# Kernel optimization log

Measured on AMD Instinct MI355X. Metric: run time of the kernel, lower is better.

## Reference

```python
import jax, jax.numpy as jnp
import numpy as np

CH = 64
GROUPS = 32
EPS = 1e-5


def setup_inputs() -> dict:
    key = jax.random.key(0)
    ks = jax.random.split(key, 10)
    b, c, h, w = 4, CH, 64, 64
    x = jax.random.normal(ks[0], (b, c, h, w), dtype=jnp.float32)
    s = 1.0 / np.sqrt(c)
    Wq = jax.random.normal(ks[1], (c, c), dtype=jnp.float32) * s
    bq = jnp.zeros((c,), dtype=jnp.float32)
    Wk = jax.random.normal(ks[2], (c, c), dtype=jnp.float32) * s
    bk = jnp.zeros((c,), dtype=jnp.float32)
    Wv = jax.random.normal(ks[3], (c, c), dtype=jnp.float32) * s
    bv = jnp.zeros((c,), dtype=jnp.float32)
    Wo = jax.random.normal(ks[4], (c, c), dtype=jnp.float32) * s
    bo = jnp.zeros((c,), dtype=jnp.float32)
    gamma = jnp.ones((c,), dtype=jnp.float32)
    beta = jnp.zeros((c,), dtype=jnp.float32)
    return {"x": x, "Wq": Wq, "bq": bq, "Wk": Wk, "bk": bk,
            "Wv": Wv, "bv": bv, "Wo": Wo, "bo": bo,
            "gamma": gamma, "beta": beta}


def group_norm(x, gamma, beta):
    b, c, h, w = x.shape
    xg = x.reshape(b, GROUPS, c // GROUPS, h, w)
    mean = jnp.mean(xg, axis=(2, 3, 4), keepdims=True)
    var = jnp.var(xg, axis=(2, 3, 4), keepdims=True)
    xn = ((xg - mean) * jax.lax.rsqrt(var + EPS)).reshape(b, c, h, w)
    return xn * gamma[None, :, None, None] + beta[None, :, None, None]


def conv1x1(x, W, bias):
    # 1x1 conv == channel matmul: x [b,c,h,w], W [out,in]
    return jnp.einsum('bchw,oc->bohw', x, W) + bias[None, :, None, None]


def reference(x, Wq, bq, Wk, bk, Wv, bv, Wo, bo, gamma, beta):
    b, c, h, w = x.shape
    n = h * w
    xn = group_norm(x, gamma, beta)
    q = conv1x1(xn, Wq, bq).reshape(b, c, n)  # [b,c,n]
    k = conv1x1(xn, Wk, bk).reshape(b, c, n)
    v = conv1x1(xn, Wv, bv).reshape(b, c, n)
    scale = 1.0 / jnp.sqrt(jnp.asarray(c, dtype=x.dtype))
    # scores: q^T k -> [b, n_q, n_k]
    attn = jax.nn.softmax(jnp.einsum('bci,bcj->bij', q, k) * scale, axis=-1)
    # out = v @ attn^T -> [b, c, n_q]
    out = jnp.einsum('bcj,bij->bci', v, attn).reshape(b, c, h, w)
    return x + conv1x1(out, Wo, bo)
```

## Files before the change

### kernel.cpp

```cpp
#include <hip/hip_runtime.h>
#include <hip/hip_bf16.h>

#define NPOS 4096
#define KS 72
#define VS 80

typedef __attribute__((ext_vector_type(4))) float f32x4;
typedef __attribute__((ext_vector_type(8))) short bf16x8;
typedef __attribute__((ext_vector_type(2))) int i32x2;
typedef _Float16 f16;
typedef __attribute__((ext_vector_type(8))) f16 f16x8;

__device__ __forceinline__ short f2bf(float f) {
  union { __hip_bfloat16 h; short s; } u;
  u.h = __float2bfloat16(f);
  return u.s;
}
__device__ __forceinline__ int pack_bf16(float lo, float hi) {
  unsigned a = (unsigned short)f2bf(lo);
  unsigned b = (unsigned short)f2bf(hi);
  return (int)(a | (b << 16));
}
__device__ __forceinline__ bf16x8 cvt8(const float* p) {
  f32x4 u = *(const f32x4*)p;
  f32x4 v = *(const f32x4*)(p + 4);
  bf16x8 r;
  r[0] = f2bf(u.x); r[1] = f2bf(u.y); r[2] = f2bf(u.z); r[3] = f2bf(u.w);
  r[4] = f2bf(v.x); r[5] = f2bf(v.y); r[6] = f2bf(v.z); r[7] = f2bf(v.w);
  return r;
}

__global__ __launch_bounds__(256) void stats_kernel(const float* __restrict__ x,
                                                    float* __restrict__ stats) {
  const int bg = blockIdx.x;
  const f32x4* base = (const f32x4*)(x + (size_t)bg * 8192);
  float s = 0.f, ss = 0.f;
  for (int i = threadIdx.x; i < 2048; i += 256) {
    f32x4 v = base[i];
    s  += v.x + v.y + v.z + v.w;
    ss += v.x * v.x + v.y * v.y + v.z * v.z + v.w * v.w;
  }
  for (int off = 32; off; off >>= 1) {
    s  += __shfl_down(s, off, 64);
    ss += __shfl_down(ss, off, 64);
  }
  __shared__ float red[8];
  const int wave = threadIdx.x >> 6, lane = threadIdx.x & 63;
  if (lane == 0) { red[wave] = s; red[4 + wave] = ss; }
  __syncthreads();
  if (threadIdx.x == 0) {
    float S  = red[0] + red[1] + red[2] + red[3];
    float SS = red[4] + red[5] + red[6] + red[7];
    float mean = S * (1.f / 8192.f);
    float var  = SS * (1.f / 8192.f) - mean * mean;
    stats[2 * bg]     = mean;
    stats[2 * bg + 1] = rsqrtf(var + 1e-5f);
  }
}

__global__ __launch_bounds__(256) void qkv_kernel(
    const float* __restrict__ x,
    const float* __restrict__ Wq, const float* __restrict__ bq,
    const float* __restrict__ Wk, const float* __restrict__ bk,
    const float* __restrict__ Wv, const float* __restrict__ bv,
    const float* __restrict__ gamma, const float* __restrict__ beta,
    const float* __restrict__ stats,
    short* __restrict__ qT, short* __restrict__ kT, short* __restrict__ vC) {
  __shared__ short xn_lds[32 * KS];
  __shared__ short out_lds[32 * 200];

  const int tid  = threadIdx.x;
  const int b    = blockIdx.x >> 7;
  const int pt   = blockIdx.x & 127;
  const int p0   = pt << 5;
  const int wave = tid >> 6;
  const int lane = tid & 63;
  const int quad = lane >> 4;
  const int l16  = lane & 15;

  bf16x8 a_lo[3], a_hi[3];
  float bias_r[3][4];
  {
    const float* Wsrc[3] = {Wq, Wk, Wv};
    const float* Bsrc[3] = {bq, bk, bv};
#pragma unroll
    for (int t = 0; t < 3; t++) {
      const float* wr = Wsrc[t] + (size_t)(wave * 16 + l16) * 64;
      a_lo[t] = cvt8(wr + quad * 8);
      a_hi[t] = cvt8(wr + 32 + quad * 8);
#pragma unroll
      for (int r = 0; r < 4; r++) bias_r[t][r] = Bsrc[t][wave * 16 + quad * 4 + r];
    }
  }

  {
    const int ch = tid >> 2, pg = tid & 3;
    float mean = stats[b * 64 + 2 * (ch >> 1)];
    float rstd = stats[b * 64 + 2 * (ch >> 1) + 1];
    float sc = rstd * gamma[ch];
    float sh = beta[ch] - mean * sc;
    const float* src = x + ((size_t)(b * 64 + ch)) * NPOS + p0 + pg * 8;
    f32x4 v0 = *(const f32x4*)src;
    f32x4 v1 = *(const f32x4*)(src + 4);
    short* d = xn_lds + ch;
    d[(pg * 8 + 0) * KS] = f2bf(fmaf(v0.x, sc, sh));
    d[(pg * 8 + 1) * KS] = f2bf(fmaf(v0.y, sc, sh));
    d[(pg * 8 + 2) * KS] = f2bf(fmaf(v0.z, sc, sh));
    d[(pg * 8 + 3) * KS] = f2bf(fmaf(v0.w, sc, sh));
    d[(pg * 8 + 4) * KS] = f2bf(fmaf(v1.x, sc, sh));
    d[(pg * 8 + 5) * KS] = f2bf(fmaf(v1.y, sc, sh));
    d[(pg * 8 + 6) * KS] = f2bf(fmaf(v1.z, sc, sh));
    d[(pg * 8 + 7) * KS] = f2bf(fmaf(v1.w, sc, sh));
  }
  __syncthreads();

  const f32x4 zero4 = {0.f, 0.f, 0.f, 0.f};
#pragma unroll
  for (int n = 0; n < 2; n++) {
    const short* xr = xn_lds + (n * 16 + l16) * KS;
    bf16x8 b_lo = *(const bf16x8*)(xr + quad * 8);
    bf16x8 b_hi = *(const bf16x8*)(xr + 32 + quad * 8);
#pragma unroll
    for (int t = 0; t < 3; t++) {
      f32x4 c = zero4;
      c = __builtin_amdgcn_mfma_f32_16x16x32_bf16(a_lo[t], b_lo, c, 0, 0, 0);
      c = __builtin_amdgcn_mfma_f32_16x16x32_bf16(a_hi[t], b_hi, c, 0, 0, 0);
      i32x2 val;
      val.x = pack_bf16(c[0] + bias_r[t][0], c[1] + bias_r[t][1]);
      val.y = pack_bf16(c[2] + bias_r[t][2], c[3] + bias_r[t][3]);
      *(i32x2*)(out_lds + (n * 16 + l16) * 200 + t * 64 + wave * 16 + quad * 4) = val;
    }
  }
  __syncthreads();

  {
    const int p = tid >> 3, c8 = (tid & 7) << 3;
    short* qd = qT + ((size_t)(b * NPOS + p0 + p)) * 64 + c8;
    *(bf16x8*)qd = *(const bf16x8*)(out_lds + p * 200 + c8);
    short* kd = kT + ((size_t)(b * NPOS + p0 + p)) * 64 + c8;
    *(bf16x8*)kd = *(const bf16x8*)(out_lds + p * 200 + 64 + c8);
  }
  {
    const int ch = tid >> 2, pg = tid & 3;
    bf16x8 v;
#pragma unroll
    for (int i = 0; i < 8; i++) v[i] = out_lds[(pg * 8 + i) * 200 + 128 + ch];
    *(bf16x8*)(vC + ((size_t)(b * 64 + ch)) * NPOS + p0 + pg * 8) = v;
  }
}

__global__ __launch_bounds__(256, 4) void flash_part_kernel(
    const short* __restrict__ qT, const short* __restrict__ kT,
    const short* __restrict__ vC, f16* __restrict__ part,
    float* __restrict__ ml) {
  __shared__ short V_lds[64 * VS];
  __shared__ short P_lds[4][32 * VS];

  const int blk   = blockIdx.x;
  const int qt    = blk & 31;
  const int chunk = (blk >> 5) & 7;
  const int b     = blk >> 8;
  const int q0    = qt << 7;
  const int jc    = chunk << 9;
  const int tid   = threadIdx.x;
  const int wave  = tid >> 6;
  const int lane  = tid & 63;
  const int quad  = lane >> 4;
  const int l16   = lane & 15;
  const float scale = 0.125f;

  bf16x8 bqf[2][2];
#pragma unroll
  for (int n = 0; n < 2; n++) {
    const short* qbase = qT + ((size_t)(b * NPOS + q0 + wave * 32 + n * 16 + l16)) * 64;
    bqf[n][0] = *(const bf16x8*)(qbase + quad * 8);
    bqf[n][1] = *(const bf16x8*)(qbase + 32 + quad * 8);
  }

  const f32x4 zero4 = {0.f, 0.f, 0.f, 0.f};
  f32x4 o_acc[2][4];
#pragma unroll
  for (int n = 0; n < 2; n++)
#pragma unroll
    for (int t = 0; t < 4; t++) o_acc[n][t] = zero4;
  float m_i[2] = {-1e30f, -1e30f}, l_i[2] = {0.f, 0.f};

  const short* kTb = kT + (size_t)b * NPOS * 64;

  for (int kt = 0; kt < 8; kt++) {
    const int j0 = jc + (kt << 6);
    __syncthreads();
    {
      const int ch = tid >> 2, go = (tid & 3) << 4;
      const bf16x8* vsrc = (const bf16x8*)(vC + ((size_t)(b * 64 + ch)) * NPOS + j0 + go);
      bf16x8* vdst = (bf16x8*)(V_lds + ch * VS + go);
      vdst[0] = vsrc[0];
      vdst[1] = vsrc[1];
    }
    __syncthreads();

    f32x4 st[2][4];
#pragma unroll
    for (int t = 0; t < 4; t++) {
      const short* kr = kTb + ((size_t)(j0 + t * 16 + l16)) * 64;
      bf16x8 ka0 = *(const bf16x8*)(kr + quad * 8);
      bf16x8 ka1 = *(const bf16x8*)(kr + 32 + quad * 8);
#pragma unroll
      for (int n = 0; n < 2; n++) {
        f32x4 acc = zero4;
        acc = __builtin_amdgcn_mfma_f32_16x16x32_bf16(ka0, bqf[n][0], acc, 0, 0, 0);
        acc = __builtin_amdgcn_mfma_f32_16x16x32_bf16(ka1, bqf[n][1], acc, 0, 0, 0);
        st[n][t] = acc;
      }
    }

#pragma unroll
    for (int n = 0; n < 2; n++) {
      float rmax = -1e30f;
#pragma unroll
      for (int t = 0; t < 4; t++)
#pragma unroll
        for (int r = 0; r < 4; r++) rmax = fmaxf(rmax, st[n][t][r]);
      rmax = fmaxf(rmax, __shfl_xor(rmax, 16, 64));
      rmax = fmaxf(rmax, __shfl_xor(rmax, 32, 64));
      float mn = fmaxf(m_i[n], rmax * scale);
      float alpha = __expf(m_i[n] - mn);
      float rsum = 0.f;
#pragma unroll
      for (int t = 0; t < 4; t++)
#pragma unroll
        for (int r = 0; r < 4; r++) {
          float pv = __expf(st[n][t][r] * scale - mn);
          st[n][t][r] = pv;
          rsum += pv;
        }
      rsum += __shfl_xor(rsum, 16, 64);
      rsum += __shfl_xor(rsum, 32, 64);
      l_i[n] = l_i[n] * alpha + rsum;
      m_i[n] = mn;
#pragma unroll
      for (int t = 0; t < 4; t++) o_acc[n][t] *= alpha;
    }

    short* pw = (short*)P_lds[wave];
#pragma unroll
    for (int n = 0; n < 2; n++)
#pragma unroll
      for (int t = 0; t < 4; t++) {
        i32x2 val;
        val.x = pack_bf16(st[n][t][0], st[n][t][1]);
        val.y = pack_bf16(st[n][t][2], st[n][t][3]);
        *(i32x2*)(pw + (n * 16 + l16) * VS + t * 16 + quad * 4) = val;
      }
    bf16x8 pb[2][2];
#pragma unroll
    for (int n = 0; n < 2; n++) {
      const short* pr = pw + (n * 16 + l16) * VS;
      pb[n][0] = *(const bf16x8*)(pr + quad * 8);
      pb[n][1] = *(const bf16x8*)(pr + 32 + quad * 8);
    }

#pragma unroll
    for (int t = 0; t < 4; t++) {
      const short* vr = V_lds + (t * 16 + l16) * VS;
      bf16x8 va0 = *(const bf16x8*)(vr + quad * 8);
      bf16x8 va1 = *(const bf16x8*)(vr + 32 + quad * 8);
#pragma unroll
      for (int n = 0; n < 2; n++) {
        o_acc[n][t] = __builtin_amdgcn_mfma_f32_16x16x32_bf16(va0, pb[n][0], o_acc[n][t], 0, 0, 0);
        o_acc[n][t] = __builtin_amdgcn_mfma_f32_16x16x32_bf16(va1, pb[n][1], o_acc[n][t], 0, 0, 0);
      }
    }
  }

  const size_t pbase = ((size_t)((b * 8 + chunk) * 32 + qt)) * 8192;
#pragma unroll
  for (int n = 0; n < 2; n++) {
    const int col = wave * 32 + n * 16 + l16;
#pragma unroll
    for (int t = 0; t < 4; t++)
#pragma unroll
      for (int r = 0; r < 4; r++)
        part[pbase + (size_t)(t * 16 + quad * 4 + r) * 128 + col] = (f16)o_acc[n][t][r];
    if (quad == 0) {
      const size_t mlbase = ((size_t)((b * 8 + chunk) * 32 + qt)) * 256;
      ml[mlbase + col]       = m_i[n];
      ml[mlbase + 128 + col] = l_i[n];
    }
  }
}

__global__ __launch_bounds__(256) void co_kernel(
    const f16* __restrict__ part, const float* __restrict__ ml,
    const float* __restrict__ Wo, const float* __restrict__ bo,
    const float* __restrict__ x, float* __restrict__ y) {
  __shared__ float sm[8][32], sl[8][32], coef[8][32];
  __shared__ short attn_lds[32 * VS];
  __shared__ float y_lds[64 * 36];

  const int tid  = threadIdx.x;
  const int b    = blockIdx.x >> 7;
  const int pt   = blockIdx.x & 127;
  const int fqt  = pt >> 2;
  const int sub  = (pt & 3) << 5;
  const int p0   = pt << 5;
  const int wave = tid >> 6;
  const int lane = tid & 63;
  const int quad = lane >> 4;
  const int l16  = lane & 15;

  const float* wr = Wo + (size_t)(wave * 16 + l16) * 64;
  bf16x8 a_lo = cvt8(wr + quad * 8);
  bf16x8 a_hi = cvt8(wr + 32 + quad * 8);

  {
    const int c = tid >> 5, r = tid & 31;
    const size_t mlbase = ((size_t)((b * 8 + c) * 32 + fqt)) * 256;
    sm[c][r] = ml[mlbase + sub + r];
    sl[c][r] = ml[mlbase + 128 + sub + r];
  }
  __syncthreads();
  if (tid < 32) {
    float ms = -1e30f;
#pragma unroll
    for (int c = 0; c < 8; c++) ms = fmaxf(ms, sm[c][tid]);
    float w[8], lt = 0.f;
#pragma unroll
    for (int c = 0; c < 8; c++) {
      w[c] = __expf(sm[c][tid] - ms);
      lt = fmaf(w[c], sl[c][tid], lt);
    }
    float inv = 1.f / lt;
#pragma unroll
    for (int c = 0; c < 8; c++) coef[c][tid] = w[c] * inv;
  }
  __syncthreads();

  {
    const int ch = tid >> 2, g = tid & 3;
    float acc[8];
#pragma unroll
    for (int i = 0; i < 8; i++) acc[i] = 0.f;
#pragma unroll
    for (int c = 0; c < 8; c++) {
      const f16x8 v = *(const f16x8*)(part +
          (((size_t)((b * 8 + c) * 32 + fqt)) * 64 + ch) * 128 + sub + g * 8);
      const float* cf = &coef[c][g * 8];
#pragma unroll
      for (int i = 0; i < 8; i++) acc[i] = fmaf(cf[i], (float)v[i], acc[i]);
    }
#pragma unroll
    for (int i = 0; i < 8; i++) attn_lds[(g * 8 + i) * VS + ch] = f2bf(acc[i]);
  }
  __syncthreads();

  const f32x4 zero4 = {0.f, 0.f, 0.f, 0.f};
#pragma unroll
  for (int n = 0; n < 2; n++) {
    const short* ar = attn_lds + (n * 16 + l16) * VS;
    bf16x8 b_lo = *(const bf16x8*)(ar + quad * 8);
    bf16x8 b_hi = *(const bf16x8*)(ar + 32 + quad * 8);
    f32x4 c = zero4;
    c = __builtin_amdgcn_mfma_f32_16x16x32_bf16(a_lo, b_lo, c, 0, 0, 0);
    c = __builtin_amdgcn_mfma_f32_16x16x32_bf16(a_hi, b_hi, c, 0, 0, 0);
#pragma unroll
    for (int r = 0; r < 4; r++)
      y_lds[(wave * 16 + quad * 4 + r) * 36 + n * 16 + l16] = c[r];
  }
  __syncthreads();

  {
    const int ch = tid >> 2, pg = tid & 3;
    const size_t off = ((size_t)(b * 64 + ch)) * NPOS + p0 + pg * 8;
    const float* xs = x + off;
    float* dst = y + off;
    float bb = bo[ch];
    const float* ys = y_lds + ch * 36 + pg * 8;
    f32x4 x0 = *(const f32x4*)xs, x1 = *(const f32x4*)(xs + 4);
    f32x4 y0 = *(const f32x4*)ys, y1 = *(const f32x4*)(ys + 4);
    f32x4 o0 = {x0.x + bb + y0.x, x0.y + bb + y0.y, x0.z + bb + y0.z, x0.w + bb + y0.w};
    f32x4 o1 = {x1.x + bb + y1.x, x1.y + bb + y1.y, x1.z + bb + y1.z, x1.w + bb + y1.w};
    *(f32x4*)dst = o0;
    *(f32x4*)(dst + 4) = o1;
  }
}

extern "C" void kernel_launch(void* const* d_in, const int* in_sizes, int n_in,
                              void* d_out, int out_size, void* d_ws, size_t ws_size,
                              hipStream_t stream) {
  const float* x     = (const float*)d_in[0];
  const float* Wq    = (const float*)d_in[1];
  const float* bq    = (const float*)d_in[2];
  const float* Wk    = (const float*)d_in[3];
  const float* bk    = (const float*)d_in[4];
  const float* Wv    = (const float*)d_in[5];
  const float* bv    = (const float*)d_in[6];
  const float* Wo    = (const float*)d_in[7];
  const float* bo    = (const float*)d_in[8];
  const float* gamma = (const float*)d_in[9];
  const float* beta  = (const float*)d_in[10];
  float* y = (float*)d_out;

  char* ws = (char*)d_ws;
  float* stats = (float*)ws;
  short* qT   = (short*)(ws + 1024);
  short* kT   = (short*)(ws + 1024 + (1u << 21));
  short* vC   = (short*)(ws + 1024 + (2u << 21));
  f16*   part = (f16*)(ws + 1024 + (3u << 21));
  float* ml   = (float*)(ws + 1024 + (11u << 21));

  stats_kernel<<<dim3(128), dim3(256), 0, stream>>>(x, stats);
  qkv_kernel<<<dim3(512), dim3(256), 0, stream>>>(x, Wq, bq, Wk, bk, Wv, bv,
                                                  gamma, beta, stats, qT, kT, vC);
  flash_part_kernel<<<dim3(1024), dim3(256), 0, stream>>>(qT, kT, vC, part, ml);
  co_kernel<<<dim3(512), dim3(256), 0, stream>>>(part, ml, Wo, bo, x, y);
}
```

Baseline: 135.9 us.

## Store V in MFMA fragment layout and load directly to registers, dropping LDS staging

The QKV kernel now writes V in a pre-swizzled per-tile fragment layout that matches the MFMA A-operand lane ordering. The flash kernel can then load V fragments straight from global memory into registers with coalesced 16-byte loads. This removes the V shared-memory buffer and the two block barriers per key tile. The cost is more global/L2 traffic per wave, since every wave reloads V, and extra register pressure from holding all V fragments during softmax.

```diff
diff --git a/kernel.cpp b/kernel.cpp
--- a/kernel.cpp
+++ b/kernel.cpp
@@ -65,7 +65,7 @@
     const float* __restrict__ Wv, const float* __restrict__ bv,
     const float* __restrict__ gamma, const float* __restrict__ beta,
     const float* __restrict__ stats,
-    short* __restrict__ qT, short* __restrict__ kT, short* __restrict__ vC) {
+    short* __restrict__ qT, short* __restrict__ kT, short* __restrict__ vF) {
   __shared__ short xn_lds[32 * KS];
   __shared__ short out_lds[32 * 200];
 
@@ -141,19 +141,23 @@
     *(bf16x8*)kd = *(const bf16x8*)(out_lds + p * 200 + 64 + c8);
   }
   {
-    const int ch = tid >> 2, pg = tid & 3;
+    const int t2  = tid >> 6;
+    const int ln  = tid & 63;
+    const int qd2 = ln >> 4, s16 = ln & 15;
     bf16x8 v;
 #pragma unroll
-    for (int i = 0; i < 8; i++) v[i] = out_lds[(pg * 8 + i) * 200 + 128 + ch];
-    *(bf16x8*)(vC + ((size_t)(b * 64 + ch)) * NPOS + p0 + pg * 8) = v;
+    for (int i = 0; i < 8; i++)
+      v[i] = out_lds[(qd2 * 8 + i) * 200 + 128 + t2 * 16 + s16];
+    const size_t base =
+        (((size_t)(b * 64 + (pt >> 1)) * 8) + t2 * 2 + (pt & 1)) * 512 + ln * 8;
+    *(bf16x8*)(vF + base) = v;
   }
 }
 
 __global__ __launch_bounds__(256, 4) void flash_part_kernel(
     const short* __restrict__ qT, const short* __restrict__ kT,
-    const short* __restrict__ vC, f16* __restrict__ part,
+    const short* __restrict__ vF, f16* __restrict__ part,
     float* __restrict__ ml) {
-  __shared__ short V_lds[64 * VS];
   __shared__ short P_lds[4][32 * VS];
 
   const int blk   = blockIdx.x;
@@ -161,7 +165,6 @@
   const int chunk = (blk >> 5) & 7;
   const int b     = blk >> 8;
   const int q0    = qt << 7;
-  const int jc    = chunk << 9;
   const int tid   = threadIdx.x;
   const int wave  = tid >> 6;
   const int lane  = tid & 63;
@@ -186,18 +189,11 @@
   float m_i[2] = {-1e30f, -1e30f}, l_i[2] = {0.f, 0.f};
 
   const short* kTb = kT + (size_t)b * NPOS * 64;
+  const short* vFb = vF + (size_t)b * 262144;
 
   for (int kt = 0; kt < 8; kt++) {
-    const int j0 = jc + (kt << 6);
-    __syncthreads();
-    {
-      const int ch = tid >> 2, go = (tid & 3) << 4;
-      const bf16x8* vsrc = (const bf16x8*)(vC + ((size_t)(b * 64 + ch)) * NPOS + j0 + go);
-      bf16x8* vdst = (bf16x8*)(V_lds + ch * VS + go);
-      vdst[0] = vsrc[0];
-      vdst[1] = vsrc[1];
-    }
-    __syncthreads();
+    const int jt = (chunk << 3) + kt;
+    const int j0 = jt << 6;
 
     f32x4 st[2][4];
 #pragma unroll
@@ -212,6 +208,14 @@
         acc = __builtin_amdgcn_mfma_f32_16x16x32_bf16(ka1, bqf[n][1], acc, 0, 0, 0);
         st[n][t] = acc;
       }
+    }
+
+    const short* vtile = vFb + (size_t)jt * 4096;
+    bf16x8 va[4][2];
+#pragma unroll
+    for (int t = 0; t < 4; t++) {
+      va[t][0] = *(const bf16x8*)(vtile + (t * 2 + 0) * 512 + lane * 8);
+      va[t][1] = *(const bf16x8*)(vtile + (t * 2 + 1) * 512 + lane * 8);
     }
 
 #pragma unroll
@@ -262,13 +266,10 @@
 
 #pragma unroll
     for (int t = 0; t < 4; t++) {
-      const short* vr = V_lds + (t * 16 + l16) * VS;
-      bf16x8 va0 = *(const bf16x8*)(vr + quad * 8);
-      bf16x8 va1 = *(const bf16x8*)(vr + 32 + quad * 8);
 #pragma unroll
       for (int n = 0; n < 2; n++) {
-        o_acc[n][t] = __builtin_amdgcn_mfma_f32_16x16x32_bf16(va0, pb[n][0], o_acc[n][t], 0, 0, 0);
-        o_acc[n][t] = __builtin_amdgcn_mfma_f32_16x16x32_bf16(va1, pb[n][1], o_acc[n][t], 0, 0, 0);
+        o_acc[n][t] = __builtin_amdgcn_mfma_f32_16x16x32_bf16(va[t][0], pb[n][0], o_acc[n][t], 0, 0, 0);
+        o_acc[n][t] = __builtin_amdgcn_mfma_f32_16x16x32_bf16(va[t][1], pb[n][1], o_acc[n][t], 0, 0, 0);
       }
     }
   }
@@ -405,13 +406,13 @@
   float* stats = (float*)ws;
   short* qT   = (short*)(ws + 1024);
   short* kT   = (short*)(ws + 1024 + (1u << 21));
-  short* vC   = (short*)(ws + 1024 + (2u << 21));
+  short* vF   = (short*)(ws + 1024 + (2u << 21));
   f16*   part = (f16*)(ws + 1024 + (3u << 21));
   float* ml   = (float*)(ws + 1024 + (11u << 21));
 
   stats_kernel<<<dim3(128), dim3(256), 0, stream>>>(x, stats);
   qkv_kernel<<<dim3(512), dim3(256), 0, stream>>>(x, Wq, bq, Wk, bk, Wv, bv,
-                                                  gamma, beta, stats, qT, kT, vC);
-  flash_part_kernel<<<dim3(1024), dim3(256), 0, stream>>>(qT, kT, vC, part, ml);
+                                                  gamma, beta, stats, qT, kT, vF);
+  flash_part_kernel<<<dim3(1024), dim3(256), 0, stream>>>(qT, kT, vF, part, ml);
   co_kernel<<<dim3(512), dim3(256), 0, stream>>>(part, ml, Wo, bo, x, y);
 }
```

Result: slower. 149.0 us (+9.7%).
